# Optimization experiments

Hardware: AMD Instinct MI355X
Metric: run time of the kernel (lower is better)

## Reference

```python
import jax, jax.numpy as jnp
import numpy as np

N_EMBD = 1024
N_HEAD = 16
D_K = N_EMBD // N_HEAD
B, T = 2, 2048
NEG = -10000000000.0


def setup_inputs() -> dict:
    key = jax.random.key(0)
    ks = jax.random.split(key, 9)
    s = 1.0 / np.sqrt(N_EMBD)
    mk = lambda k: jax.random.uniform(k, (N_EMBD, N_EMBD), jnp.float32, -s, s)
    mb = lambda k: jax.random.uniform(k, (N_EMBD,), jnp.float32, -s, s)
    return {
        "x": jax.random.normal(ks[0], (B, T, N_EMBD), jnp.float32),
        "Wq": mk(ks[1]), "bq": mb(ks[2]),
        "Wk": mk(ks[3]), "bk": mb(ks[4]),
        "Wv": mk(ks[5]), "bv": mb(ks[6]),
        "Wo": mk(ks[7]), "bo": mb(ks[8]),
    }


def reference(x, Wq, bq, Wk, bk, Wv, bv, Wo, bo):
    Bx, Tx, _ = x.shape
    split = lambda h: h.reshape(Bx, Tx, N_HEAD, D_K).transpose(0, 2, 1, 3)  # [B,H,T,d_k]
    q = split(x @ Wq.T + bq)
    k = split(x @ Wk.T + bk)
    v = split(x @ Wv.T + bv)
    scores = jnp.einsum("bhqd,bhkd->bhqk", q, k) / np.sqrt(D_K)
    causal = jnp.tril(jnp.ones((Tx, Tx), dtype=bool))
    scores = jnp.where(causal[None, None], scores, NEG)
    prob = jax.nn.softmax(scores, axis=-1)
    y = jnp.einsum("bhqk,bhkd->bhqd", prob, v)
    y = y.transpose(0, 2, 1, 3).reshape(Bx, Tx, N_EMBD)
    return y @ Wo.T + bo
```

## Files before the change

kernel.cpp:

```cpp
#include <hip/hip_runtime.h>
#include <hip/hip_bf16.h>

#define N_EMBD 1024
#define T_SEQ  2048
#define BATCH  2
#define NHEAD  16
#define DKH    64
#define MTOK   (BATCH * T_SEQ)

typedef __attribute__((ext_vector_type(8))) short short8;
typedef __attribute__((ext_vector_type(4))) short short4v;
typedef __attribute__((ext_vector_type(4))) float floatx4;

#define QSCALE 0.18033688011112042f

static __device__ __forceinline__ short bf16_of(float f) {
    union { float f; unsigned u; } x; x.f = f;
    unsigned r = (x.u + 0x7fff + ((x.u >> 16) & 1)) >> 16;
    return (short)r;
}


__global__ __launch_bounds__(256) void cvt_frag(
    const float* __restrict__ x,  const float* __restrict__ Wq,
    const float* __restrict__ Wk, const float* __restrict__ Wv,
    const float* __restrict__ Wo,
    short* __restrict__ xf, short* __restrict__ wqkf,
    short* __restrict__ wvf, short* __restrict__ wof)
{
    int b = blockIdx.x;
    const float* src; short* dst; int srb, drb;
    if (b < 256)      { src = x;  dst = xf;   srb = b;       drb = srb; }
    else if (b < 320) { src = Wq; dst = wqkf; srb = b - 256; drb = srb; }
    else if (b < 384) { src = Wk; dst = wqkf; srb = b - 320; drb = srb + 64; }
    else if (b < 448) { src = Wv; dst = wvf;  srb = b - 384; drb = srb; }
    else              { src = Wo; dst = wof;  srb = b - 448; drb = srb; }

    const int row16 = threadIdx.x >> 4;
    const int kseg  = (threadIdx.x & 15) * 64;
    const float* sp = src + ((long)srb * 16 + row16) * 1024 + kseg;
    short* dp       = dst + ((long)drb * 32 + (kseg >> 5)) * 512 + row16 * 8;

#pragma unroll
    for (int c = 0; c < 8; ++c) {
        float4 v0 = *(const float4*)(sp + c * 8);
        float4 v1 = *(const float4*)(sp + c * 8 + 4);
        short8 o;
        o[0] = bf16_of(v0.x); o[1] = bf16_of(v0.y); o[2] = bf16_of(v0.z); o[3] = bf16_of(v0.w);
        o[4] = bf16_of(v1.x); o[5] = bf16_of(v1.y); o[6] = bf16_of(v1.z); o[7] = bf16_of(v1.w);
        *(short8*)(dp + (c >> 2) * 512 + (c & 3) * 128) = o;
    }
}

#define GEMM_KLOOP(Ab, Bb)                                                     \
    floatx4 acc[4][8] = {};                                                    \
    short8 a0[4], a1[4], b0[8], b1[8];                                         \
    _Pragma("unroll") for (int i = 0; i < 4; ++i)                              \
        a0[i] = *(const short8*)(Ab + (long)i * 32 * 512);                     \
    _Pragma("unroll") for (int j = 0; j < 8; ++j)                              \
        b0[j] = *(const short8*)(Bb + (long)j * 32 * 512);                     \
    for (int kc = 0; kc < 32; kc += 2) {                                       \
        _Pragma("unroll") for (int i = 0; i < 4; ++i)                          \
            a1[i] = *(const short8*)(Ab + ((long)i * 32 + kc + 1) * 512);      \
        _Pragma("unroll") for (int j = 0; j < 8; ++j)                          \
            b1[j] = *(const short8*)(Bb + ((long)j * 32 + kc + 1) * 512);      \
        _Pragma("unroll") for (int i = 0; i < 4; ++i)                          \
            _Pragma("unroll") for (int j = 0; j < 8; ++j)                      \
                acc[i][j] = __builtin_amdgcn_mfma_f32_16x16x32_bf16(           \
                    a0[i], b0[j], acc[i][j], 0, 0, 0);                         \
        if (kc + 2 < 32) {                                                     \
            _Pragma("unroll") for (int i = 0; i < 4; ++i)                      \
                a0[i] = *(const short8*)(Ab + ((long)i * 32 + kc + 2) * 512);  \
            _Pragma("unroll") for (int j = 0; j < 8; ++j)                      \
                b0[j] = *(const short8*)(Bb + ((long)j * 32 + kc + 2) * 512);  \
        }                                                                      \
        _Pragma("unroll") for (int i = 0; i < 4; ++i)                          \
            _Pragma("unroll") for (int j = 0; j < 8; ++j)                      \
                acc[i][j] = __builtin_amdgcn_mfma_f32_16x16x32_bf16(           \
                    a1[i], b1[j], acc[i][j], 0, 0, 0);                         \
    }

__global__ __launch_bounds__(64, 2) void gemm_qkv(
    const short* __restrict__ xf, const short* __restrict__ wqkf,
    const short* __restrict__ wvf,
    const float* __restrict__ bq, const float* __restrict__ bk, const float* __restrict__ bv,
    short* __restrict__ outQ, short* __restrict__ outK, short* __restrict__ outV)
{
    const int lane = threadIdx.x & 63;
    const int quad = lane >> 4, lr = lane & 15;
    const int wid  = blockIdx.x;
    const bool isQK = wid < 1024;
    int mw, nw;
    const short *Af, *Bf;
    if (isQK) { mw = (wid >> 5) * 64;          nw = (wid & 31) * 128; Af = wqkf; Bf = xf; }
    else      { int v = wid - 1024;
                mw = (v >> 3) * 64;            nw = (v & 7) * 128;    Af = xf;   Bf = wvf; }

    const short* Ab = Af + (long)(mw >> 4) * 32 * 512 + lane * 8;
    const short* Bb = Bf + (long)(nw >> 4) * 32 * 512 + lane * 8;

    GEMM_KLOOP(Ab, Bb)

    if (isQK) {
#pragma unroll
        for (int i = 0; i < 4; ++i) {
#pragma unroll
            for (int j = 0; j < 8; ++j) {
                int f0  = mw + i * 16 + quad * 4;
                int t   = nw + j * 16 + lr;
                int tb  = t & 2047;
                int sel = f0 >> 10;
                int fb  = f0 & 1023;
                int h   = fb >> 6, d0 = fb & 63;
                long bh = (long)(t >> 11) * NHEAD + h;
                float4 bias = *(const float4*)((sel ? bk : bq) + fb);
                short4v y;
#pragma unroll
                for (int r = 0; r < 4; ++r) {
                    float v = acc[i][j][r] + (&bias.x)[r];
                    if (sel == 0) v *= QSCALE;
                    y[r] = bf16_of(v);
                }
                long idx = ((bh * 128 + (tb >> 4)) * 2 + (d0 >> 5)) * 512
                         + (((d0 >> 3) & 3) * 16 + (tb & 15)) * 8 + (d0 & 7);
                *(short4v*)((sel ? outK : outQ) + idx) = y;
            }
        }
    } else {
#pragma unroll
        for (int i = 0; i < 4; ++i) {
#pragma unroll
            for (int j = 0; j < 8; ++j) {
                int t0 = mw + i * 16 + quad * 4;
                int tb = t0 & 2047;
                int d  = nw + j * 16 + lr;
                int h  = d >> 6, dblk = (d >> 4) & 3;
                long bh = (long)(t0 >> 11) * NHEAD + h;
                float bias = bv[d];
                short4v y;
#pragma unroll
                for (int r = 0; r < 4; ++r) y[r] = bf16_of(acc[i][j][r] + bias);
                long idx = ((bh * 64 + (tb >> 5)) * 4 + dblk) * 512
                         + lane * 8 + (i & 1) * 4;
                *(short4v*)(outV + idx) = y;
            }
        }
    }
}

__global__ __launch_bounds__(64, 2) void gemm_proj(
    const short* __restrict__ Yf, const short* __restrict__ wof,
    const float* __restrict__ bo, float* __restrict__ out)
{
    const int lane = threadIdx.x & 63;
    const int quad = lane >> 4, lr = lane & 15;
    const int wid  = blockIdx.x;
    const int mw   = (wid >> 5) * 64;
    const int nw   = (wid & 31) * 128;

    const short* Ab = wof + (long)(mw >> 4) * 32 * 512 + lane * 8;
    const short* Bb = Yf  + (long)(nw >> 4) * 32 * 512 + lane * 8;

    GEMM_KLOOP(Ab, Bb)

#pragma unroll
    for (int i = 0; i < 4; ++i) {
#pragma unroll
        for (int j = 0; j < 8; ++j) {
            int  f0 = mw + i * 16 + quad * 4;
            long t  = nw + j * 16 + lr;
            float4 b4 = *(const float4*)(bo + f0);
            float4 o4;
            o4.x = acc[i][j][0] + b4.x;
            o4.y = acc[i][j][1] + b4.y;
            o4.z = acc[i][j][2] + b4.z;
            o4.w = acc[i][j][3] + b4.w;
            *(float4*)(out + t * N_EMBD + f0) = o4;
        }
    }
}

__global__ __launch_bounds__(256) void attn_kernel(
    const short* __restrict__ Qf, const short* __restrict__ Kf,
    const short* __restrict__ Vf, short* __restrict__ Y)
{
    __shared__ float Ob[2][32][68];
    __shared__ float Lb[2][32];

    const int tid  = threadIdx.x;
    const int w    = tid >> 6, lane = tid & 63;
    const int quad = lane >> 4, lr = lane & 15;
    const int qs   = w & 1, half = w >> 1;

    const int id = blockIdx.x;
    const int qt = 31 - (id >> 5);
    const int bh = id & 31;

    const short* Qp = Qf + (long)bh * 131072;
    const short* Kp = Kf + (long)bh * 131072;
    const short* Vp = Vf + (long)bh * 131072;

    const int qrb = qt * 64 + qs * 32;
    const int qb  = qrb >> 4;

    short8 qfv[2][2];
#pragma unroll
    for (int m = 0; m < 2; ++m)
#pragma unroll
        for (int c = 0; c < 2; ++c)
            qfv[m][c] = *(const short8*)(Qp + (long)(((qb + m) * 2 + c) * 512) + lane * 8);

    floatx4 o[2][4] = {};
    float rs[2] = {0.f, 0.f};

    const int S_tot = 2 * qt + qs + 1;
    const int h0 = (S_tot + 1) >> 1;
    const int sb = half ? h0 : 0;
    const int se = half ? S_tot : h0;

    short8 kbn[2][2];
    if (sb < se) {
#pragma unroll
        for (int blk = 0; blk < 2; ++blk)
#pragma unroll
            for (int c = 0; c < 2; ++c)
                kbn[blk][c] = *(const short8*)(Kp + (long)(((sb * 2 + blk) * 2 + c) * 512) + lane * 8);
    }

    for (int s = sb; s < se; ++s) {
        short8 ka[2][2];
#pragma unroll
        for (int blk = 0; blk < 2; ++blk)
#pragma unroll
            for (int c = 0; c < 2; ++c) ka[blk][c] = kbn[blk][c];
        if (s + 1 < se) {
#pragma unroll
            for (int blk = 0; blk < 2; ++blk)
#pragma unroll
                for (int c = 0; c < 2; ++c)
                    kbn[blk][c] = *(const short8*)(Kp + (long)((((s + 1) * 2 + blk) * 2 + c) * 512) + lane * 8);
        }
        short8 va[4];
#pragma unroll
        for (int d = 0; d < 4; ++d)
            va[d] = *(const short8*)(Vp + (long)((s * 4 + d) * 512) + lane * 8);

        floatx4 sc[2][2];
#pragma unroll
        for (int m = 0; m < 2; ++m)
#pragma unroll
            for (int blk = 0; blk < 2; ++blk) {
                floatx4 z = {};
                z = __builtin_amdgcn_mfma_f32_16x16x32_bf16(ka[blk][0], qfv[m][0], z, 0, 0, 0);
                z = __builtin_amdgcn_mfma_f32_16x16x32_bf16(ka[blk][1], qfv[m][1], z, 0, 0, 0);
                sc[m][blk] = z;
            }

        if (s == S_tot - 1) {
            const int k0 = s * 32;
#pragma unroll
            for (int m = 0; m < 2; ++m)
#pragma unroll
                for (int blk = 0; blk < 2; ++blk)
#pragma unroll
                    for (int r = 0; r < 4; ++r) {
                        int key = k0 + blk * 16 + quad * 4 + r;
                        if (key > qrb + m * 16 + lr) sc[m][blk][r] = -INFINITY;
                    }
        }

        short8 pa[2];
#pragma unroll
        for (int m = 0; m < 2; ++m) {
            union { short8 v; short e[8]; } pu;
#pragma unroll
            for (int blk = 0; blk < 2; ++blk)
#pragma unroll
                for (int r = 0; r < 4; ++r) {
                    float p = __builtin_amdgcn_exp2f(sc[m][blk][r]);
                    rs[m] += p;
                    union { float f; unsigned u; } cc; cc.f = p;
                    pu.e[blk * 4 + r] = (short)((cc.u + 0x8000u) >> 16);
                }
            pa[m] = pu.v;
        }

#pragma unroll
        for (int m = 0; m < 2; ++m)
#pragma unroll
            for (int d = 0; d < 4; ++d)
                o[m][d] = __builtin_amdgcn_mfma_f32_16x16x32_bf16(va[d], pa[m], o[m][d], 0, 0, 0);
    }

#pragma unroll
    for (int m = 0; m < 2; ++m) {
        rs[m] += __shfl_xor(rs[m], 16, 64);
        rs[m] += __shfl_xor(rs[m], 32, 64);
    }

    if (half == 1) {
#pragma unroll
        for (int m = 0; m < 2; ++m) {
#pragma unroll
            for (int d = 0; d < 4; ++d)
                *(floatx4*)&Ob[qs][m * 16 + lr][d * 16 + quad * 4] = o[m][d];
            Lb[qs][m * 16 + lr] = rs[m];
        }
    }
    __syncthreads();
    if (half == 0) {
        const long rb0 = (long)(bh >> 4) * 128 + qb;
        const int  hk  = (bh & 15) * DKH;
#pragma unroll
        for (int m = 0; m < 2; ++m) {
            float l   = rs[m] + Lb[qs][m * 16 + lr];
            float inv = 1.f / l;
            long  rb  = rb0 + m;
#pragma unroll
            for (int d = 0; d < 4; ++d) {
                floatx4 ob = *(const floatx4*)&Ob[qs][m * 16 + lr][d * 16 + quad * 4];
                short4v y4;
#pragma unroll
                for (int r = 0; r < 4; ++r) y4[r] = bf16_of((o[m][d][r] + ob[r]) * inv);
                int kb = hk + d * 16 + quad * 4;
                long idx = (rb * 32 + (kb >> 5)) * 512
                         + (((kb >> 3) & 3) * 16 + lr) * 8 + (quad & 1) * 4;
                *(short4v*)(Y + idx) = y4;
            }
        }
    }
}

extern "C" void kernel_launch(void* const* d_in, const int* in_sizes, int n_in,
                              void* d_out, int out_size, void* d_ws, size_t ws_size,
                              hipStream_t stream) {
    const float* x  = (const float*)d_in[0];
    const float* Wq = (const float*)d_in[1];
    const float* bq = (const float*)d_in[2];
    const float* Wk = (const float*)d_in[3];
    const float* bk = (const float*)d_in[4];
    const float* Wv = (const float*)d_in[5];
    const float* bv = (const float*)d_in[6];
    const float* Wo = (const float*)d_in[7];
    const float* bo = (const float*)d_in[8];
    float* out = (float*)d_out;

    char* ws = (char*)d_ws;
    short* xf   = (short*)(ws);
    short* wqkf = (short*)(ws + (8L  << 20));
    short* wvf  = (short*)(ws + (12L << 20));
    short* wof  = (short*)(ws + (14L << 20));
    short* Qb   = (short*)(ws + (16L << 20));
    short* Kbuf = (short*)(ws + (24L << 20));
    short* Vtb  = (short*)(ws + (32L << 20));
    short* Yf   = xf;

    cvt_frag<<<512, 256, 0, stream>>>(x, Wq, Wk, Wv, Wo, xf, wqkf, wvf, wof);

    gemm_qkv<<<1536, 64, 0, stream>>>(xf, wqkf, wvf, bq, bk, bv, Qb, Kbuf, Vtb);
    attn_kernel<<<1024, 256, 0, stream>>>(Qb, Kbuf, Vtb, Yf);
    gemm_proj<<<512, 64, 0, stream>>>(Yf, wof, bo, out);
}
```

Baseline: 171.0 us.

## Pair GEMM waves per block with barrier sync; prefetch V and raise MFMA priority

The GEMM kernels now launch two waves per block, each taking an adjacent 64-row M tile that shares the same B columns. A per-iteration barrier keeps the two waves in lockstep so their shared B loads hit cache together. The attention kernel now double-buffers V loads alongside K, and raises wave priority around its MFMA sections with s_setprio. The barrier adds sync cost in exchange for better cache reuse, and the prefetch uses more registers.

```diff
diff --git a/kernel.cpp b/kernel.cpp
--- a/kernel.cpp
+++ b/kernel.cpp
@@ -60,6 +60,7 @@
     _Pragma("unroll") for (int j = 0; j < 8; ++j)                              \
         b0[j] = *(const short8*)(Bb + (long)j * 32 * 512);                     \
     for (int kc = 0; kc < 32; kc += 2) {                                       \
+        __builtin_amdgcn_s_barrier();                                          \
         _Pragma("unroll") for (int i = 0; i < 4; ++i)                          \
             a1[i] = *(const short8*)(Ab + ((long)i * 32 + kc + 1) * 512);      \
         _Pragma("unroll") for (int j = 0; j < 8; ++j)                          \
@@ -80,21 +81,22 @@
                     a1[i], b1[j], acc[i][j], 0, 0, 0);                         \
     }
 
-__global__ __launch_bounds__(64, 2) void gemm_qkv(
+__global__ __launch_bounds__(128, 2) void gemm_qkv(
     const short* __restrict__ xf, const short* __restrict__ wqkf,
     const short* __restrict__ wvf,
     const float* __restrict__ bq, const float* __restrict__ bk, const float* __restrict__ bv,
     short* __restrict__ outQ, short* __restrict__ outK, short* __restrict__ outV)
 {
     const int lane = threadIdx.x & 63;
+    const int w    = threadIdx.x >> 6;
     const int quad = lane >> 4, lr = lane & 15;
-    const int wid  = blockIdx.x;
-    const bool isQK = wid < 1024;
+    const int bid  = blockIdx.x;
+    const bool isQK = bid < 512;
     int mw, nw;
     const short *Af, *Bf;
-    if (isQK) { mw = (wid >> 5) * 64;          nw = (wid & 31) * 128; Af = wqkf; Bf = xf; }
-    else      { int v = wid - 1024;
-                mw = (v >> 3) * 64;            nw = (v & 7) * 128;    Af = xf;   Bf = wvf; }
+    if (isQK) { mw = ((bid >> 5) * 2 + w) * 64;  nw = (bid & 31) * 128; Af = wqkf; Bf = xf; }
+    else      { int v = bid - 512;
+                mw = ((v >> 3) * 2 + w) * 64;    nw = (v & 7) * 128;    Af = xf;   Bf = wvf; }
 
     const short* Ab = Af + (long)(mw >> 4) * 32 * 512 + lane * 8;
     const short* Bb = Bf + (long)(nw >> 4) * 32 * 512 + lane * 8;
@@ -148,15 +150,16 @@
     }
 }
 
-__global__ __launch_bounds__(64, 2) void gemm_proj(
+__global__ __launch_bounds__(128, 2) void gemm_proj(
     const short* __restrict__ Yf, const short* __restrict__ wof,
     const float* __restrict__ bo, float* __restrict__ out)
 {
     const int lane = threadIdx.x & 63;
+    const int w    = threadIdx.x >> 6;
     const int quad = lane >> 4, lr = lane & 15;
-    const int wid  = blockIdx.x;
-    const int mw   = (wid >> 5) * 64;
-    const int nw   = (wid & 31) * 128;
+    const int bid  = blockIdx.x;
+    const int mw   = ((bid >> 5) * 2 + w) * 64;
+    const int nw   = (bid & 31) * 128;
 
     const short* Ab = wof + (long)(mw >> 4) * 32 * 512 + lane * 8;
     const short* Bb = Yf  + (long)(nw >> 4) * 32 * 512 + lane * 8;
@@ -219,33 +222,41 @@
     const int se = half ? S_tot : h0;
 
     short8 kbn[2][2];
+    short8 vbn[4];
     if (sb < se) {
 #pragma unroll
         for (int blk = 0; blk < 2; ++blk)
 #pragma unroll
             for (int c = 0; c < 2; ++c)
                 kbn[blk][c] = *(const short8*)(Kp + (long)(((sb * 2 + blk) * 2 + c) * 512) + lane * 8);
+#pragma unroll
+        for (int d = 0; d < 4; ++d)
+            vbn[d] = *(const short8*)(Vp + (long)((sb * 4 + d) * 512) + lane * 8);
     }
 
     for (int s = sb; s < se; ++s) {
         short8 ka[2][2];
+        short8 va[4];
 #pragma unroll
         for (int blk = 0; blk < 2; ++blk)
 #pragma unroll
             for (int c = 0; c < 2; ++c) ka[blk][c] = kbn[blk][c];
+#pragma unroll
+        for (int d = 0; d < 4; ++d) va[d] = vbn[d];
+
         if (s + 1 < se) {
 #pragma unroll
             for (int blk = 0; blk < 2; ++blk)
 #pragma unroll
                 for (int c = 0; c < 2; ++c)
                     kbn[blk][c] = *(const short8*)(Kp + (long)((((s + 1) * 2 + blk) * 2 + c) * 512) + lane * 8);
-        }
-        short8 va[4];
-#pragma unroll
-        for (int d = 0; d < 4; ++d)
-            va[d] = *(const short8*)(Vp + (long)((s * 4 + d) * 512) + lane * 8);
+#pragma unroll
+            for (int d = 0; d < 4; ++d)
+                vbn[d] = *(const short8*)(Vp + (long)(((s + 1) * 4 + d) * 512) + lane * 8);
+        }
 
         floatx4 sc[2][2];
+        __builtin_amdgcn_s_setprio(1);
 #pragma unroll
         for (int m = 0; m < 2; ++m)
 #pragma unroll
@@ -255,6 +266,7 @@
                 z = __builtin_amdgcn_mfma_f32_16x16x32_bf16(ka[blk][1], qfv[m][1], z, 0, 0, 0);
                 sc[m][blk] = z;
             }
+        __builtin_amdgcn_s_setprio(0);
 
         if (s == S_tot - 1) {
             const int k0 = s * 32;
@@ -285,11 +297,13 @@
             pa[m] = pu.v;
         }
 
+        __builtin_amdgcn_s_setprio(1);
 #pragma unroll
         for (int m = 0; m < 2; ++m)
 #pragma unroll
             for (int d = 0; d < 4; ++d)
                 o[m][d] = __builtin_amdgcn_mfma_f32_16x16x32_bf16(va[d], pa[m], o[m][d], 0, 0, 0);
+        __builtin_amdgcn_s_setprio(0);
     }
 
 #pragma unroll
@@ -357,7 +371,7 @@
 
     cvt_frag<<<512, 256, 0, stream>>>(x, Wq, Wk, Wv, Wo, xf, wqkf, wvf, wof);
 
-    gemm_qkv<<<1536, 64, 0, stream>>>(xf, wqkf, wvf, bq, bk, bv, Qb, Kbuf, Vtb);
+    gemm_qkv<<<768, 128, 0, stream>>>(xf, wqkf, wvf, bq, bk, bv, Qb, Kbuf, Vtb);
     attn_kernel<<<1024, 256, 0, stream>>>(Qb, Kbuf, Vtb, Yf);
-    gemm_proj<<<512, 64, 0, stream>>>(Yf, wof, bo, out);
-}
+    gemm_proj<<<256, 128, 0, stream>>>(Yf, wof, bo, out);
+}
```

New measurement: 174.5 us. +2.1%, slower.
